# Performance work log

Measured on AMD Instinct MI355X. Metric: run time of the kernel, lower is better.

Reference implementation:

```python
import jax, jax.numpy as jnp
import numpy as np

N_NODES = 100000
N_EDGES = 1200000
D_IN = 64
D_OUT = 64


def setup_inputs() -> dict:
    key = jax.random.key(0)
    ks = jax.random.split(key, 8)
    feat = jax.random.normal(ks[0], (N_NODES, D_IN), dtype=jnp.float32)
    src = jax.random.randint(ks[1], (N_EDGES,), 0, N_NODES, dtype=jnp.int32)
    dst = jax.random.randint(ks[2], (N_EDGES,), 0, N_NODES, dtype=jnp.int32)
    edge_weight = jax.random.uniform(ks[3], (N_EDGES, 1), dtype=jnp.float32)
    edge_mask = jax.random.uniform(ks[4], (N_EDGES, 1), dtype=jnp.float32)
    W_self = jax.random.normal(ks[5], (D_OUT, D_IN), dtype=jnp.float32) * (1.0 / np.sqrt(D_IN))
    b_self = jnp.zeros((D_OUT,), dtype=jnp.float32)
    W_neigh = jax.random.normal(ks[6], (D_OUT, D_IN), dtype=jnp.float32) * (1.0 / np.sqrt(D_IN))
    b_neigh = jnp.zeros((D_OUT,), dtype=jnp.float32)
    return {"feat": feat, "src": src, "dst": dst, "edge_weight": edge_weight,
            "edge_mask": edge_mask, "W_self": W_self, "b_self": b_self,
            "W_neigh": W_neigh, "b_neigh": b_neigh}


def reference(feat, src, dst, edge_weight, edge_mask, W_self, b_self, W_neigh, b_neigh):
    # message: gather src feats, scale by per-edge weight and mask  -> [E, D_IN]
    msg = feat[src] * edge_weight * edge_mask
    # mean scatter-reduce over incoming edges per dst node
    neigh_sum = jax.ops.segment_sum(msg, dst, num_segments=N_NODES)  # [N, D_IN]
    deg = jax.ops.segment_sum(jnp.ones((msg.shape[0],), dtype=feat.dtype), dst,
                              num_segments=N_NODES)  # [N]
    h_neigh = neigh_sum / jnp.maximum(deg, 1.0)[:, None]  # zero-degree nodes -> 0 (DGL mean semantics)
    # dual linear fuse
    rst = (feat @ W_self.T + b_self) + (h_neigh @ W_neigh.T + b_neigh)
    return rst
```

## Files before the change

### kernel.cpp

```cpp
#include <hip/hip_runtime.h>

#define NB_MAX   1568
#define CAP      1024
#define BT_EDGES 5120
#define BT_TPB   1024
#define EPE      5

typedef __attribute__((ext_vector_type(4))) float floatx4;
typedef __attribute__((ext_vector_type(2))) float floatx2;
typedef __attribute__((ext_vector_type(8))) short bf16x8;
typedef __attribute__((ext_vector_type(4))) unsigned uintx4;

__device__ __forceinline__ unsigned short f32_to_bf16(float f) {
  unsigned u = __float_as_uint(f);
  u = (u + 0x7fffu + ((u >> 16) & 1u)) >> 16;
  return (unsigned short)u;
}
__device__ __forceinline__ unsigned pack2(float a, float b) {
  return (unsigned)f32_to_bf16(a) | ((unsigned)f32_to_bf16(b) << 16);
}
__device__ __forceinline__ bf16x8 zero_bf16x8() {
  bf16x8 v;
#pragma unroll
  for (int i = 0; i < 8; ++i) v[i] = 0;
  return v;
}

#if __has_builtin(__builtin_amdgcn_cvt_pk_fp8_f32)
__device__ __forceinline__ unsigned pack_fp8x4(float a, float b, float c, float d) {
  unsigned v = (unsigned)__builtin_amdgcn_cvt_pk_fp8_f32(a, b, 0, false);
  v = (unsigned)__builtin_amdgcn_cvt_pk_fp8_f32(c, d, (int)v, true);
  return v;
}
#else
__device__ __forceinline__ unsigned sw_f32_fp8(float f) {
  unsigned u = __float_as_uint(f);
  unsigned s = (u >> 24) & 0x80u;
  unsigned au = u & 0x7fffffffu;
  if (au > 0x43E00000u) au = 0x43E00000u;
  au += 0x7FFFFu + ((au >> 20) & 1u);
  int e = (int)(au >> 23) - 120;
  if (e <= 0) return s;
  return s | ((unsigned)e << 3) | ((au >> 20) & 7u);
}
__device__ __forceinline__ unsigned pack_fp8x4(float a, float b, float c, float d) {
  return sw_f32_fp8(a) | (sw_f32_fp8(b) << 8) | (sw_f32_fp8(c) << 16) |
         (sw_f32_fp8(d) << 24);
}
#endif

#if __has_builtin(__builtin_amdgcn_cvt_pk_f32_fp8)
__device__ __forceinline__ void dec4(float* acc, unsigned w32, float wt) {
  floatx2 f0 = __builtin_amdgcn_cvt_pk_f32_fp8((int)w32, false);
  floatx2 f1 = __builtin_amdgcn_cvt_pk_f32_fp8((int)w32, true);
  acc[0] += wt * f0.x; acc[1] += wt * f0.y;
  acc[2] += wt * f1.x; acc[3] += wt * f1.y;
}
#else
__device__ __forceinline__ float sw_fp8_f32(unsigned b) {
  unsigned s = (b & 0x80u) << 24;
  unsigned e = (b >> 3) & 0xFu;
  unsigned m = b & 7u;
  float fn = __uint_as_float(s | ((e + 120u) << 23) | (m << 20));
  float fd = (float)(int)m * 0.001953125f;
  fd = (b & 0x80u) ? -fd : fd;
  return e ? fn : fd;
}
__device__ __forceinline__ void dec4(float* acc, unsigned w32, float wt) {
  acc[0] += wt * sw_fp8_f32(w32 & 0xFF);
  acc[1] += wt * sw_fp8_f32((w32 >> 8) & 0xFF);
  acc[2] += wt * sw_fp8_f32((w32 >> 16) & 0xFF);
  acc[3] += wt * sw_fp8_f32(w32 >> 24);
}
#endif

__global__ __launch_bounds__(BT_TPB) void k_build(
    const float* __restrict__ feat, const int* __restrict__ src,
    const int* __restrict__ dst, const float* __restrict__ ew,
    const float* __restrict__ em, const float* __restrict__ Ws,
    const float* __restrict__ Wn, int* __restrict__ gCursor,
    unsigned* __restrict__ recs, unsigned short* __restrict__ featb,
    unsigned char* __restrict__ featq, unsigned short* __restrict__ Wb,
    int E, int nChunks, int nB) {
  __shared__ unsigned stage[BT_EDGES];
  __shared__ unsigned short stageB[BT_EDGES];
  __shared__ int A[NB_MAX];
  __shared__ int B[NB_MAX];
  __shared__ int waveSums[16];

  const int t = threadIdx.x;
  const int lane = t & 63;
  const int wvid = t >> 6;
  const int e0 = blockIdx.x * BT_EDGES;
  const int eEnd = min(e0 + BT_EDGES, E);
  const int nLocal = eEnd - e0;

  for (int i = t; i < NB_MAX; i += BT_TPB) B[i] = 0;
  __syncthreads();

  int dreg[EPE];
  unsigned rreg[EPE];
#pragma unroll
  for (int k = 0; k < EPE; ++k) {
    int i = e0 + k * BT_TPB + t;
    dreg[k] = -1;
    if (i < eEnd) {
      int d = __builtin_nontemporal_load(&dst[i]);
      dreg[k] = d;
      atomicAdd(&B[d >> 6], 1);
      float w = __builtin_nontemporal_load(&ew[i]) *
                __builtin_nontemporal_load(&em[i]);
      int wq = (int)(w * 511.0f + 0.5f);
      if (wq > 511) wq = 511;
      rreg[k] = (unsigned)__builtin_nontemporal_load(&src[i]) |
                ((unsigned)(d & 63) << 17) | ((unsigned)wq << 23);
    }
  }
  __syncthreads();

  {
    const int EPT = 2;
    int b0 = t * EPT;
    int v[EPT];
    int sum = 0;
#pragma unroll
    for (int j = 0; j < EPT; ++j) {
      v[j] = (b0 + j < nB) ? B[b0 + j] : 0;
      sum += v[j];
    }
    int x = sum;
#pragma unroll
    for (int d = 1; d < 64; d <<= 1) {
      int y = __shfl_up(x, d, 64);
      if (lane >= d) x += y;
    }
    if (lane == 63) waveSums[wvid] = x;
    __syncthreads();
    int wprefix = 0;
    for (int i = 0; i < wvid; ++i) wprefix += waveSums[i];
    int run = wprefix + x - sum;
#pragma unroll
    for (int j = 0; j < EPT; ++j) {
      if (b0 + j < nB) A[b0 + j] = run;
      run += v[j];
    }
  }
  __syncthreads();

  for (int i = t; i < nB; i += BT_TPB) {
    int c = B[i];
    int l = A[i];
    int g = c ? atomicAdd(&gCursor[i], c) : 0;
    A[i] = i * CAP + g - l;
    B[i] = l;
  }
  __syncthreads();

#pragma unroll
  for (int k = 0; k < EPE; ++k) {
    if (dreg[k] >= 0) {
      int bkt = dreg[k] >> 6;
      int r = atomicAdd(&B[bkt], 1);
      stage[r] = rreg[k];
      stageB[r] = (unsigned short)bkt;
    }
  }
  __syncthreads();

  for (int i = t; i < nLocal; i += BT_TPB) {
    int bkt = stageB[i];
    int pos = A[bkt] + i;
    if (pos < (bkt + 1) * CAP)
      recs[pos] = stage[i];
  }

  const size_t PL = (size_t)nChunks * 4;
  for (int c = blockIdx.x * BT_TPB + t; c < nChunks; c += gridDim.x * BT_TPB) {
    const floatx4* fp = reinterpret_cast<const floatx4*>(feat) + (size_t)c * 2;
    floatx4 a = __builtin_nontemporal_load(fp);
    floatx4 b = __builtin_nontemporal_load(fp + 1);
    uintx4 o;
    o.x = pack2(a.x, a.y);
    o.y = pack2(a.z, a.w);
    o.z = pack2(b.x, b.y);
    o.w = pack2(b.z, b.w);
    __builtin_nontemporal_store(o, reinterpret_cast<uintx4*>(featb) + c);
    uint2 q8;
    q8.x = pack_fp8x4(a.x, a.y, a.z, a.w);
    q8.y = pack_fp8x4(b.x, b.y, b.z, b.w);
    int n = c >> 3, h = (c >> 2) & 1, j = c & 3;
    reinterpret_cast<uint2*>(featq + (size_t)h * PL)[(size_t)n * 4 + j] = q8;
  }

  if (blockIdx.x == 0) {
    for (int i = t; i < 1024; i += BT_TPB) {
      int j = i >> 4, c4 = i & 15;
      float4 w4 = reinterpret_cast<const float4*>(Ws)[i];
      float4 n4 = reinterpret_cast<const float4*>(Wn)[i];
      *reinterpret_cast<uint2*>(&Wb[j * 128 + c4 * 4]) =
          make_uint2(pack2(w4.x, w4.y), pack2(w4.z, w4.w));
      *reinterpret_cast<uint2*>(&Wb[j * 128 + 64 + c4 * 4]) =
          make_uint2(pack2(n4.x, n4.y), pack2(n4.z, n4.w));
    }
  }
}

__global__ __launch_bounds__(256, 8) void sage_gather_gemm(
    const unsigned short* __restrict__ featb,
    const unsigned char* __restrict__ featq,
    const unsigned short* __restrict__ Wb, const int* __restrict__ gCursor,
    const unsigned* __restrict__ recs, const float* __restrict__ bs,
    const float* __restrict__ bn, float* __restrict__ out, int N) {
  __shared__ unsigned short An[64][72];
  __shared__ unsigned rawL[CAP];
  __shared__ unsigned srtL[CAP];
  __shared__ int cntS[64], offS[64], curS[64];

  const int t = threadIdx.x;
  const int b = blockIdx.x;
  const int n0 = b * 64;
  const int base = b * CAP;
  const int cb = min(gCursor[b], CAP);

  if (t < 64) cntS[t] = 0;
  __syncthreads();

  for (int i = t; i < cb; i += 256) {
    unsigned r = __builtin_nontemporal_load(&recs[base + i]);
    rawL[i] = r;
    atomicAdd(&cntS[(r >> 17) & 63], 1);
  }
  __syncthreads();

  if (t < 64) {
    int c = cntS[t];
    int x = c;
#pragma unroll
    for (int d = 1; d < 64; d <<= 1) {
      int y = __shfl_up(x, d, 64);
      if (t >= d) x += y;
    }
    offS[t] = x - c;
    curS[t] = x - c;
  }
  __syncthreads();

  for (int i = t; i < cb; i += 256) {
    unsigned r = rawL[i];
    int p = atomicAdd(&curS[(r >> 17) & 63], 1);
    srtL[p] = r;
  }
  __syncthreads();

  const int wv = t >> 6;
  const int ln = t & 63;
  const int col = ln & 15;
  const int quad = ln >> 4;
  const int gn = n0 + wv * 16 + col;
  bf16x8 af0 = zero_bf16x8(), af1 = zero_bf16x8();

  {
    const int nl = t >> 2;
    const int q  = t & 3;
    const int deg = cntS[nl], off = offS[nl];
    float acc[16];
#pragma unroll
    for (int i = 0; i < 16; ++i) acc[i] = 0.f;
    const uint2* fq0 = reinterpret_cast<const uint2*>(featq);
    const uint2* fq1 =
        reinterpret_cast<const uint2*>(featq + (size_t)N * 32);

#define GPHASE(FQ, A0, A1)                                   \
    {                                                        \
      uint2 uC = {0, 0}, uN = {0, 0};                        \
      float wC = 0.f, wN = 0.f;                              \
      if (deg > 0) {                                         \
        unsigned r0 = srtL[off];                             \
        uC = FQ[(size_t)(r0 & 0x1FFFF) * 4 + q];             \
        wC = (float)(r0 >> 23) * (1.0f / 511.0f);            \
      }                                                      \
      if (deg > 1) {                                         \
        unsigned r1 = srtL[off + 1];                         \
        uN = FQ[(size_t)(r1 & 0x1FFFF) * 4 + q];             \
        wN = (float)(r1 >> 23) * (1.0f / 511.0f);            \
      }                                                      \
      for (int m = 0; m < deg; ++m) {                        \
        uint2 u = uC;                                        \
        float w = wC;                                        \
        uC = uN; wC = wN;                                    \
        if (m + 2 < deg) {                                   \
          unsigned rn = srtL[off + m + 2];                   \
          uN = FQ[(size_t)(rn & 0x1FFFF) * 4 + q];           \
          wN = (float)(rn >> 23) * (1.0f / 511.0f);          \
        }                                                    \
        dec4(acc + (A0), u.x, w);                            \
        dec4(acc + (A1), u.y, w);                            \
      }                                                      \
    }
    GPHASE(fq0, 0, 4)
    GPHASE(fq1, 8, 12)
#undef GPHASE

    float inv = 1.0f / fmaxf((float)deg, 1.0f);
#pragma unroll
    for (int i = 0; i < 16; ++i) acc[i] *= inv;
    uint4 o0, o1;
    o0.x = pack2(acc[0], acc[1]);
    o0.y = pack2(acc[2], acc[3]);
    o0.z = pack2(acc[4], acc[5]);
    o0.w = pack2(acc[6], acc[7]);
    o1.x = pack2(acc[8], acc[9]);
    o1.y = pack2(acc[10], acc[11]);
    o1.z = pack2(acc[12], acc[13]);
    o1.w = pack2(acc[14], acc[15]);
    *reinterpret_cast<uint4*>(&An[nl][q * 8]) = o0;
    *reinterpret_cast<uint4*>(&An[nl][32 + q * 8]) = o1;
  }

  if (gn < N) {
    af0 = __builtin_nontemporal_load(
        reinterpret_cast<const bf16x8*>(featb + (size_t)gn * 64 + quad * 8));
    af1 = __builtin_nontemporal_load(
        reinterpret_cast<const bf16x8*>(featb + (size_t)gn * 64 + 32 + quad * 8));
  }
  floatx4 acc4[4];
#pragma unroll
  for (int jt = 0; jt < 4; ++jt) {
    float bb = bs[jt * 16 + col] + bn[jt * 16 + col];
    acc4[jt] = (floatx4){bb, bb, bb, bb};
  }
  __syncthreads();

#pragma unroll
  for (int kk = 0; kk < 4; ++kk) {
    bf16x8 af;
    if (kk == 0)      af = af0;
    else if (kk == 1) af = af1;
    else
      af = *reinterpret_cast<const bf16x8*>(
          &An[wv * 16 + col][(kk - 2) * 32 + quad * 8]);
#pragma unroll
    for (int jt = 0; jt < 4; ++jt) {
      bf16x8 bf = *reinterpret_cast<const bf16x8*>(
          Wb + (jt * 16 + col) * 128 + kk * 32 + quad * 8);
      acc4[jt] = __builtin_amdgcn_mfma_f32_16x16x32_bf16(af, bf, acc4[jt], 0, 0, 0);
    }
  }

#pragma unroll
  for (int jt = 0; jt < 4; ++jt) {
#pragma unroll
    for (int r = 0; r < 4; ++r) {
      int m = quad * 4 + r;
      int g2 = n0 + wv * 16 + m;
      if (g2 < N)
        __builtin_nontemporal_store(acc4[jt][r],
                                    &out[(size_t)g2 * 64 + jt * 16 + col]);
    }
  }
}

extern "C" void kernel_launch(void* const* d_in, const int* in_sizes, int n_in,
                              void* d_out, int out_size, void* d_ws, size_t ws_size,
                              hipStream_t stream) {
  const float* feat = (const float*)d_in[0];
  const int*   src  = (const int*)d_in[1];
  const int*   dst  = (const int*)d_in[2];
  const float* ew   = (const float*)d_in[3];
  const float* em   = (const float*)d_in[4];
  const float* Ws   = (const float*)d_in[5];
  const float* bs   = (const float*)d_in[6];
  const float* Wn   = (const float*)d_in[7];
  const float* bn   = (const float*)d_in[8];
  float* out = (float*)d_out;

  const int N = in_sizes[0] / 64;
  const int E = in_sizes[1];
  const int nB = (N + 63) / 64;

  unsigned short* featb = (unsigned short*)d_ws;
  unsigned char*  featq = (unsigned char*)(featb + (size_t)N * 64);
  unsigned short* Wb    = (unsigned short*)(featq + (size_t)N * 64);
  unsigned* recs   = (unsigned*)(Wb + 64 * 128);
  int*      gCursor = (int*)(recs + (size_t)NB_MAX * CAP);

  hipMemsetAsync(gCursor, 0, NB_MAX * sizeof(int), stream);

  int nChunks = N * 8;
  int gB = (E + BT_EDGES - 1) / BT_EDGES;

  k_build<<<gB, BT_TPB, 0, stream>>>(feat, src, dst, ew, em, Ws, Wn,
                                     gCursor, recs, featb, featq, Wb,
                                     E, nChunks, nB);
  sage_gather_gemm<<<nB, 256, 0, stream>>>(featb, featq, Wb, gCursor, recs,
                                           bs, bn, out, N);
}
```

Baseline: 162.7 us.

## Gather full fp8 rows in one pass with source-half edge ordering

The fp8 feature copy is now stored row-contiguous (64 bytes per node) instead of split into two 32-byte planes. Each thread gathers 16 bytes per edge in a single walk rather than two walks over 8 bytes each. Edges within a destination are also sub-sorted by whether the source index falls in the lower or upper half of the node range, which aims to improve cache locality of the gathers. The cost is wider per-lane loads and doubled shared-memory counters and scan bookkeeping, with a changed column mapping when packing into An.

Measured after the change: 156.9 us. 3.6% less time.

```diff
diff --git a/kernel.cpp b/kernel.cpp
--- a/kernel.cpp
+++ b/kernel.cpp
@@ -174,7 +174,6 @@
       recs[pos] = stage[i];
   }
 
-  const size_t PL = (size_t)nChunks * 4;
   for (int c = blockIdx.x * BT_TPB + t; c < nChunks; c += gridDim.x * BT_TPB) {
     const floatx4* fp = reinterpret_cast<const floatx4*>(feat) + (size_t)c * 2;
     floatx4 a = __builtin_nontemporal_load(fp);
@@ -188,8 +187,7 @@
     uint2 q8;
     q8.x = pack_fp8x4(a.x, a.y, a.z, a.w);
     q8.y = pack_fp8x4(b.x, b.y, b.z, b.w);
-    int n = c >> 3, h = (c >> 2) & 1, j = c & 3;
-    reinterpret_cast<uint2*>(featq + (size_t)h * PL)[(size_t)n * 4 + j] = q8;
+    reinterpret_cast<uint2*>(featq)[c] = q8;
   }
 
   if (blockIdx.x == 0) {
@@ -214,40 +212,47 @@
   __shared__ unsigned short An[64][72];
   __shared__ unsigned rawL[CAP];
   __shared__ unsigned srtL[CAP];
-  __shared__ int cntS[64], offS[64], curS[64];
+  __shared__ int cntS[128], offS[128], curS[128];
 
   const int t = threadIdx.x;
   const int b = blockIdx.x;
   const int n0 = b * 64;
   const int base = b * CAP;
   const int cb = min(gCursor[b], CAP);
-
-  if (t < 64) cntS[t] = 0;
+  const unsigned half = (unsigned)(N >> 1);
+
+  if (t < 128) cntS[t] = 0;
   __syncthreads();
 
   for (int i = t; i < cb; i += 256) {
     unsigned r = __builtin_nontemporal_load(&recs[base + i]);
     rawL[i] = r;
-    atomicAdd(&cntS[(r >> 17) & 63], 1);
+    int key = (int)(((r >> 17) & 63) << 1) + (int)((r & 0x1FFFFu) >= half);
+    atomicAdd(&cntS[key], 1);
   }
   __syncthreads();
 
   if (t < 64) {
-    int c = cntS[t];
-    int x = c;
+    int v0 = cntS[2 * t], v1 = cntS[2 * t + 1];
+    int sum = v0 + v1;
+    int x = sum;
 #pragma unroll
     for (int d = 1; d < 64; d <<= 1) {
       int y = __shfl_up(x, d, 64);
       if (t >= d) x += y;
     }
-    offS[t] = x - c;
-    curS[t] = x - c;
+    int e0 = x - sum;
+    offS[2 * t] = e0;
+    offS[2 * t + 1] = e0 + v0;
+    curS[2 * t] = e0;
+    curS[2 * t + 1] = e0 + v0;
   }
   __syncthreads();
 
   for (int i = t; i < cb; i += 256) {
     unsigned r = rawL[i];
-    int p = atomicAdd(&curS[(r >> 17) & 63], 1);
+    int key = (int)(((r >> 17) & 63) << 1) + (int)((r & 0x1FFFFu) >= half);
+    int p = atomicAdd(&curS[key], 1);
     srtL[p] = r;
   }
   __syncthreads();
@@ -262,44 +267,46 @@
   {
     const int nl = t >> 2;
     const int q  = t & 3;
-    const int deg = cntS[nl], off = offS[nl];
+    const int degA = cntS[2 * nl], offA = offS[2 * nl];
+    const int degB = cntS[2 * nl + 1], offB = offS[2 * nl + 1];
+    const int deg = degA + degB;
     float acc[16];
 #pragma unroll
     for (int i = 0; i < 16; ++i) acc[i] = 0.f;
-    const uint2* fq0 = reinterpret_cast<const uint2*>(featq);
-    const uint2* fq1 =
-        reinterpret_cast<const uint2*>(featq + (size_t)N * 32);
-
-#define GPHASE(FQ, A0, A1)                                   \
+    const uint4* fq = reinterpret_cast<const uint4*>(featq);
+
+#define GWALK(OFF, DEG)                                      \
     {                                                        \
-      uint2 uC = {0, 0}, uN = {0, 0};                        \
+      uint4 uC = {0, 0, 0, 0}, uN = {0, 0, 0, 0};            \
       float wC = 0.f, wN = 0.f;                              \
-      if (deg > 0) {                                         \
-        unsigned r0 = srtL[off];                             \
-        uC = FQ[(size_t)(r0 & 0x1FFFF) * 4 + q];             \
+      if ((DEG) > 0) {                                       \
+        unsigned r0 = srtL[(OFF)];                           \
+        uC = fq[(size_t)(r0 & 0x1FFFF) * 4 + q];             \
         wC = (float)(r0 >> 23) * (1.0f / 511.0f);            \
       }                                                      \
-      if (deg > 1) {                                         \
-        unsigned r1 = srtL[off + 1];                         \
-        uN = FQ[(size_t)(r1 & 0x1FFFF) * 4 + q];             \
+      if ((DEG) > 1) {                                       \
+        unsigned r1 = srtL[(OFF) + 1];                       \
+        uN = fq[(size_t)(r1 & 0x1FFFF) * 4 + q];             \
         wN = (float)(r1 >> 23) * (1.0f / 511.0f);            \
       }                                                      \
-      for (int m = 0; m < deg; ++m) {                        \
-        uint2 u = uC;                                        \
+      for (int m = 0; m < (DEG); ++m) {                      \
+        uint4 u = uC;                                        \
         float w = wC;                                        \
         uC = uN; wC = wN;                                    \
-        if (m + 2 < deg) {                                   \
-          unsigned rn = srtL[off + m + 2];                   \
-          uN = FQ[(size_t)(rn & 0x1FFFF) * 4 + q];           \
+        if (m + 2 < (DEG)) {                                 \
+          unsigned rn = srtL[(OFF) + m + 2];                 \
+          uN = fq[(size_t)(rn & 0x1FFFF) * 4 + q];           \
           wN = (float)(rn >> 23) * (1.0f / 511.0f);          \
         }                                                    \
-        dec4(acc + (A0), u.x, w);                            \
-        dec4(acc + (A1), u.y, w);                            \
+        dec4(acc + 0, u.x, w);                               \
+        dec4(acc + 4, u.y, w);                               \
+        dec4(acc + 8, u.z, w);                               \
+        dec4(acc + 12, u.w, w);                              \
       }                                                      \
     }
-    GPHASE(fq0, 0, 4)
-    GPHASE(fq1, 8, 12)
-#undef GPHASE
+    GWALK(offA, degA)
+    GWALK(offB, degB)
+#undef GWALK
 
     float inv = 1.0f / fmaxf((float)deg, 1.0f);
 #pragma unroll
@@ -313,8 +320,8 @@
     o1.y = pack2(acc[10], acc[11]);
     o1.z = pack2(acc[12], acc[13]);
     o1.w = pack2(acc[14], acc[15]);
-    *reinterpret_cast<uint4*>(&An[nl][q * 8]) = o0;
-    *reinterpret_cast<uint4*>(&An[nl][32 + q * 8]) = o1;
+    *reinterpret_cast<uint4*>(&An[nl][q * 16]) = o0;
+    *reinterpret_cast<uint4*>(&An[nl][q * 16 + 8]) = o1;
   }
 
   if (gn < N) {
```
